# Kernel optimization log

Measured on AMD Instinct MI355X. Metric: run time of the kernel, lower is better.

## Reference

```python
import jax, jax.numpy as jnp
import numpy as np

GROUP_SIZE = 7
ROI_SCALE = 1.3
BIN_SCALE = 1.5


def setup_inputs() -> dict:
    key = jax.random.key(0)
    k1, k2, k3, k4 = jax.random.split(key, 4)
    B, C, H, W = 2, 490, 128, 128  # C = output_dim(10) * group_size(7)**2
    N = 512
    stride = 16
    features = jax.random.normal(k1, (B, C, H, W), dtype=jnp.float32)
    img_w = W * stride
    bidx = jax.random.randint(k2, (N, 1), 0, B).astype(jnp.float32)
    xy1 = jax.random.uniform(k3, (N, 2), minval=0.0, maxval=img_w - 64.0)
    wh = jax.random.uniform(k4, (N, 2), minval=32.0, maxval=512.0)
    xy2 = jnp.minimum(xy1 + wh, img_w - 1.0)
    rois = jnp.concatenate([bidx, xy1[:, 0:1], xy1[:, 1:2], xy2[:, 0:1], xy2[:, 1:2]], axis=1)
    return {"rois": rois, "features": features, "stride": stride}


def reference(rois, features, stride):
    G = GROUP_SIZE
    B, C, H, W = features.shape
    D = C // (G * G)  # output_dim, computed dynamically as in the torch module
    dt = features.dtype
    spatial_scale = 1.0 / stride

    rois = rois[:, :5].astype(dt)
    batch_idx = rois[:, 0].astype(jnp.int32)  # [N]
    # rounded roi corners in feature-map coordinates (end is inclusive +1)
    rsw = jnp.round(rois[:, 1]) * spatial_scale
    rsh = jnp.round(rois[:, 2]) * spatial_scale
    rew = (jnp.round(rois[:, 3]) + 1.0) * spatial_scale
    reh = (jnp.round(rois[:, 4]) + 1.0) * spatial_scale
    # mask (context) enlargement around roi center by ROI_SCALE
    rw, rh = rew - rsw, reh - rsh
    rwm, rhm = rw * ROI_SCALE, rh * ROI_SCALE
    swm = (rsw + rew) * 0.5 - rwm * 0.5
    shm = (rsh + reh) * 0.5 - rhm * 0.5
    rwm = jnp.maximum(rwm, 0.1)  # force tiny rois to 1x1
    rhm = jnp.maximum(rhm, 0.1)
    bin_h = rhm / G  # [N]
    bin_w = rwm / G
    dh = bin_h * (BIN_SCALE - 1.0) * 0.5  # extra bin context
    dw = bin_w * (BIN_SCALE - 1.0) * 0.5

    g = jnp.arange(G, dtype=dt)  # bin index
    hstart = jnp.clip(jnp.floor(shm[:, None] + g[None, :] * bin_h[:, None] - dh[:, None]), 0, H).astype(jnp.int32)  # [N,G]
    hend = jnp.clip(jnp.ceil(shm[:, None] + (g[None, :] + 1.0) * bin_h[:, None] + dh[:, None]), 0, H).astype(jnp.int32)
    wstart = jnp.clip(jnp.floor(swm[:, None] + g[None, :] * bin_w[:, None] - dw[:, None]), 0, W).astype(jnp.int32)
    wend = jnp.clip(jnp.ceil(swm[:, None] + (g[None, :] + 1.0) * bin_w[:, None] + dw[:, None]), 0, W).astype(jnp.int32)

    # integral image so each bin-average is 4 gathers instead of a dynamic loop
    cs = jnp.cumsum(jnp.cumsum(features, axis=2), axis=3)
    S = jnp.pad(cs, ((0, 0), (0, 0), (1, 0), (1, 0)))  # [B,C,H+1,W+1]
    # position-sensitive channel map c = (d*G + ph)*G + pw  <=>  reshape C -> [D,G,G]
    Sr = S.reshape(B, D, G, G, H + 1, W + 1)

    N = rois.shape[0]
    b_ = batch_idx[:, None, None, None]          # [N,1,1,1]
    d_ = jnp.arange(D)[None, :, None, None]      # [1,D,1,1]
    pi = jnp.arange(G)[None, None, :, None]      # [1,1,G,1] (ph)
    pj = jnp.arange(G)[None, None, None, :]      # [1,1,1,G] (pw)
    hs = hstart[:, None, :, None]
    he = hend[:, None, :, None]
    ws = wstart[:, None, None, :]
    we = wend[:, None, None, :]

    total = (Sr[b_, d_, pi, pj, he, we] - Sr[b_, d_, pi, pj, hs, we]
             - Sr[b_, d_, pi, pj, he, ws] + Sr[b_, d_, pi, pj, hs, ws])  # [N,D,G,G]

    area = ((hend - hstart)[:, None, :, None] * (wend - wstart)[:, None, None, :])  # [N,1->D,G,G] via broadcast
    area = jnp.broadcast_to(area, total.shape)
    out = jnp.where(area > 0, total / jnp.maximum(area, 1).astype(dt), jnp.zeros((), dt))
    return out
```

## Files before the change

### kernel.cpp

```cpp
#include <hip/hip_runtime.h>

#define GS   7
#define CCH  490
#define HH   128
#define WW   128
#define LDW  132
#define NB   2

__global__ __launch_bounds__(512, 4) void psroi_fused(
    const float* __restrict__ rois,
    const float* __restrict__ feat,
    const int*   __restrict__ stride_p,
    float*       __restrict__ out)
{
#pragma clang fp contract(off)
    __shared__ float S[HH * LDW];

    const int bc = blockIdx.x;
    const int b  = bc / CCH;
    const int c  = bc - b * CCH;
    const float* __restrict__ f = feat + (size_t)bc * (HH * WW);
    const int tid = threadIdx.x;

    {
        const int col = tid & 127;
        const int seg = tid >> 7;
        const int r0  = seg * 32;

        float v[32];
        const float* fp = f + r0 * WW + col;
        #pragma unroll
        for (int i = 0; i < 32; ++i)
            v[i] = fp[i * WW];
        #pragma unroll
        for (int i = 1; i < 32; ++i)
            v[i] += v[i - 1];

        S[seg * LDW + col] = v[31];
        __syncthreads();
        float off = 0.0f;
        if (seg > 0) off += S[0 * LDW + col];
        if (seg > 1) off += S[1 * LDW + col];
        if (seg > 2) off += S[2 * LDW + col];
        __syncthreads();

        float* sp = &S[r0 * LDW + col];
        #pragma unroll
        for (int i = 0; i < 32; ++i)
            sp[i * LDW] = v[i] + off;
    }
    __syncthreads();

    {
        const int row = tid >> 2;
        const int ws_ = tid & 3;
        float* rp = &S[row * LDW + ws_ * 32];

        float u[32];
        #pragma unroll
        for (int i = 0; i < 8; ++i) {
            const float4 q = *(const float4*)&rp[i * 4];
            u[4 * i + 0] = q.x; u[4 * i + 1] = q.y;
            u[4 * i + 2] = q.z; u[4 * i + 3] = q.w;
        }
        #pragma unroll
        for (int i = 1; i < 32; ++i)
            u[i] += u[i - 1];

        const float tot = u[31];
        const float t1 = __shfl_up(tot, 1, 64);
        const float t2 = __shfl_up(tot, 2, 64);
        const float t3 = __shfl_up(tot, 3, 64);
        float off = 0.0f;
        if (ws_ > 0) off += t1;
        if (ws_ > 1) off += t2;
        if (ws_ > 2) off += t3;

        #pragma unroll
        for (int i = 0; i < 8; ++i) {
            float4 q;
            q.x = u[4 * i + 0] + off; q.y = u[4 * i + 1] + off;
            q.z = u[4 * i + 2] + off; q.w = u[4 * i + 3] + off;
            *(float4*)&rp[i * 4] = q;
        }
    }
    __syncthreads();

    {
        const int n = tid;
        const float b_f = rois[n * 5 + 0];
        const int bi = (int)b_f;
        if (bi == b) {
            const float ss = 1.0f / (float)(*stride_p);
            const int d   = c / (GS * GS);
            const int rem = c - d * (GS * GS);
            const int pi  = rem / GS;
            const int pj  = rem - pi * GS;

            const float x1 = rois[n * 5 + 1];
            const float y1 = rois[n * 5 + 2];
            const float x2 = rois[n * 5 + 3];
            const float y2 = rois[n * 5 + 4];

            float rsw = rintf(x1) * ss;
            float rsh = rintf(y1) * ss;
            float rew = (rintf(x2) + 1.0f) * ss;
            float reh = (rintf(y2) + 1.0f) * ss;
            float rwv = rew - rsw;
            float rhv = reh - rsh;
            float rwm = rwv * 1.3f;
            float rhm = rhv * 1.3f;
            float swm = (rsw + rew) * 0.5f - rwm * 0.5f;
            float shm = (rsh + reh) * 0.5f - rhm * 0.5f;
            rwm = fmaxf(rwm, 0.1f);
            rhm = fmaxf(rhm, 0.1f);
            float bin_h = rhm / 7.0f;
            float bin_w = rwm / 7.0f;
            float dh = bin_h * 0.25f;
            float dw = bin_w * 0.25f;

            const float gi = (float)pi;
            const float gj = (float)pj;
            const int hs  = (int)fminf(fmaxf(floorf(shm + gi * bin_h - dh),          0.0f), 128.0f);
            const int he  = (int)fminf(fmaxf(ceilf (shm + (gi + 1.0f) * bin_h + dh), 0.0f), 128.0f);
            const int ws2 = (int)fminf(fmaxf(floorf(swm + gj * bin_w - dw),          0.0f), 128.0f);
            const int we  = (int)fminf(fmaxf(ceilf (swm + (gj + 1.0f) * bin_w + dw), 0.0f), 128.0f);

            const int area = (he - hs) * (we - ws2);
            const float A  = (he > 0 && we  > 0) ? S[(he - 1) * LDW + (we  - 1)] : 0.0f;
            const float Bv = (hs > 0 && we  > 0) ? S[(hs - 1) * LDW + (we  - 1)] : 0.0f;
            const float Cv = (he > 0 && ws2 > 0) ? S[(he - 1) * LDW + (ws2 - 1)] : 0.0f;
            const float Dv = (hs > 0 && ws2 > 0) ? S[(hs - 1) * LDW + (ws2 - 1)] : 0.0f;
            const float total = ((A - Bv) - Cv) + Dv;
            out[(size_t)n * CCH + c] = (area > 0) ? (total / (float)area) : 0.0f;
        }
    }
}

extern "C" void kernel_launch(void* const* d_in, const int* in_sizes, int n_in,
                              void* d_out, int out_size, void* d_ws, size_t ws_size,
                              hipStream_t stream)
{
    const float* rois     = (const float*)d_in[0];
    const float* feat     = (const float*)d_in[1];
    const int*   stride_p = (const int*)d_in[2];
    float*       out      = (float*)d_out;

    dim3 grid(NB * CCH);
    dim3 block(512);
    hipLaunchKernelGGL(psroi_fused, grid, block, 0, stream, rois, feat, stride_p, out);
}
```

Before: 97.78 us.

## Process both batch images per block and prefetch second image during first

Each block now handles one channel for both batch images instead of one (channel, batch) pair, halving the grid to 490 blocks. The second image's column loads are issued into registers while the first image's integral image is finished and pooled, so global loads overlap LDS work. ROI geometry is computed once and reused for both batches, and __syncthreads is replaced by an lgkmcnt wait plus a raw s_barrier. The risk is lower parallelism: 490 blocks of 512 threads may underfill the GPU, and register pressure rises because the prefetched values stay live.

```diff
diff --git a/kernel.cpp b/kernel.cpp
--- a/kernel.cpp
+++ b/kernel.cpp
@@ -5,7 +5,12 @@
 #define HH   128
 #define WW   128
 #define LDW  132
-#define NB   2
+#define HWSZ (HH * WW)
+
+__device__ __forceinline__ void bar_lds() {
+    asm volatile("s_waitcnt lgkmcnt(0)" ::: "memory");
+    __builtin_amdgcn_s_barrier();
+}
 
 __global__ __launch_bounds__(512, 4) void psroi_fused(
     const float* __restrict__ rois,
@@ -16,42 +21,65 @@
 #pragma clang fp contract(off)
     __shared__ float S[HH * LDW];
 
-    const int bc = blockIdx.x;
-    const int b  = bc / CCH;
-    const int c  = bc - b * CCH;
-    const float* __restrict__ f = feat + (size_t)bc * (HH * WW);
+    const int c   = blockIdx.x;
     const int tid = threadIdx.x;
 
+    const int col = tid & 127;
+    const int seg = tid >> 7;
+    const int r0  = seg * 32;
+
+    const float* __restrict__ f0 = feat + (size_t)c * HWSZ;
+    const float* __restrict__ f1 = feat + (size_t)(CCH + c) * HWSZ;
+
+    float v[32];
     {
-        const int col = tid & 127;
-        const int seg = tid >> 7;
-        const int r0  = seg * 32;
-
-        float v[32];
-        const float* fp = f + r0 * WW + col;
+        const float* fp = f0 + r0 * WW + col;
         #pragma unroll
         for (int i = 0; i < 32; ++i)
             v[i] = fp[i * WW];
-        #pragma unroll
-        for (int i = 1; i < 32; ++i)
-            v[i] += v[i - 1];
+    }
 
-        S[seg * LDW + col] = v[31];
-        __syncthreads();
-        float off = 0.0f;
-        if (seg > 0) off += S[0 * LDW + col];
-        if (seg > 1) off += S[1 * LDW + col];
-        if (seg > 2) off += S[2 * LDW + col];
-        __syncthreads();
+    const int n = tid;
+    const float b_f = rois[n * 5 + 0];
+    const int   bi  = (int)b_f;
+    const float ss  = 1.0f / (float)(*stride_p);
+    const int d   = c / (GS * GS);
+    const int rem = c - d * (GS * GS);
+    const int pi  = rem / GS;
+    const int pj  = rem - pi * GS;
 
-        float* sp = &S[r0 * LDW + col];
-        #pragma unroll
-        for (int i = 0; i < 32; ++i)
-            sp[i * LDW] = v[i] + off;
-    }
-    __syncthreads();
+    const float x1 = rois[n * 5 + 1];
+    const float y1 = rois[n * 5 + 2];
+    const float x2 = rois[n * 5 + 3];
+    const float y2 = rois[n * 5 + 4];
 
-    {
+    float rsw = rintf(x1) * ss;
+    float rsh = rintf(y1) * ss;
+    float rew = (rintf(x2) + 1.0f) * ss;
+    float reh = (rintf(y2) + 1.0f) * ss;
+    float rwv = rew - rsw;
+    float rhv = reh - rsh;
+    float rwm = rwv * 1.3f;
+    float rhm = rhv * 1.3f;
+    float swm = (rsw + rew) * 0.5f - rwm * 0.5f;
+    float shm = (rsh + reh) * 0.5f - rhm * 0.5f;
+    rwm = fmaxf(rwm, 0.1f);
+    rhm = fmaxf(rhm, 0.1f);
+    float bin_h = rhm / 7.0f;
+    float bin_w = rwm / 7.0f;
+    float dh = bin_h * 0.25f;
+    float dw = bin_w * 0.25f;
+
+    const float gi = (float)pi;
+    const float gj = (float)pj;
+    const int hs  = (int)fminf(fmaxf(floorf(shm + gi * bin_h - dh),          0.0f), 128.0f);
+    const int he  = (int)fminf(fmaxf(ceilf (shm + (gi + 1.0f) * bin_h + dh), 0.0f), 128.0f);
+    const int ws2 = (int)fminf(fmaxf(floorf(swm + gj * bin_w - dw),          0.0f), 128.0f);
+    const int we  = (int)fminf(fmaxf(ceilf (swm + (gj + 1.0f) * bin_w + dw), 0.0f), 128.0f);
+    const int area = (he - hs) * (we - ws2);
+
+    auto phaseB = [&]() {
+#pragma clang fp contract(off)
         const int row = tid >> 2;
         const int ws_ = tid & 3;
         float* rp = &S[row * LDW + ws_ * 32];
@@ -71,62 +99,23 @@
         const float t1 = __shfl_up(tot, 1, 64);
         const float t2 = __shfl_up(tot, 2, 64);
         const float t3 = __shfl_up(tot, 3, 64);
-        float off = 0.0f;
-        if (ws_ > 0) off += t1;
-        if (ws_ > 1) off += t2;
-        if (ws_ > 2) off += t3;
+        float off2 = 0.0f;
+        if (ws_ > 0) off2 += t1;
+        if (ws_ > 1) off2 += t2;
+        if (ws_ > 2) off2 += t3;
 
         #pragma unroll
         for (int i = 0; i < 8; ++i) {
             float4 q;
-            q.x = u[4 * i + 0] + off; q.y = u[4 * i + 1] + off;
-            q.z = u[4 * i + 2] + off; q.w = u[4 * i + 3] + off;
+            q.x = u[4 * i + 0] + off2; q.y = u[4 * i + 1] + off2;
+            q.z = u[4 * i + 2] + off2; q.w = u[4 * i + 3] + off2;
             *(float4*)&rp[i * 4] = q;
         }
-    }
-    __syncthreads();
+    };
 
-    {
-        const int n = tid;
-        const float b_f = rois[n * 5 + 0];
-        const int bi = (int)b_f;
-        if (bi == b) {
-            const float ss = 1.0f / (float)(*stride_p);
-            const int d   = c / (GS * GS);
-            const int rem = c - d * (GS * GS);
-            const int pi  = rem / GS;
-            const int pj  = rem - pi * GS;
-
-            const float x1 = rois[n * 5 + 1];
-            const float y1 = rois[n * 5 + 2];
-            const float x2 = rois[n * 5 + 3];
-            const float y2 = rois[n * 5 + 4];
-
-            float rsw = rintf(x1) * ss;
-            float rsh = rintf(y1) * ss;
-            float rew = (rintf(x2) + 1.0f) * ss;
-            float reh = (rintf(y2) + 1.0f) * ss;
-            float rwv = rew - rsw;
-            float rhv = reh - rsh;
-            float rwm = rwv * 1.3f;
-            float rhm = rhv * 1.3f;
-            float swm = (rsw + rew) * 0.5f - rwm * 0.5f;
-            float shm = (rsh + reh) * 0.5f - rhm * 0.5f;
-            rwm = fmaxf(rwm, 0.1f);
-            rhm = fmaxf(rhm, 0.1f);
-            float bin_h = rhm / 7.0f;
-            float bin_w = rwm / 7.0f;
-            float dh = bin_h * 0.25f;
-            float dw = bin_w * 0.25f;
-
-            const float gi = (float)pi;
-            const float gj = (float)pj;
-            const int hs  = (int)fminf(fmaxf(floorf(shm + gi * bin_h - dh),          0.0f), 128.0f);
-            const int he  = (int)fminf(fmaxf(ceilf (shm + (gi + 1.0f) * bin_h + dh), 0.0f), 128.0f);
-            const int ws2 = (int)fminf(fmaxf(floorf(swm + gj * bin_w - dw),          0.0f), 128.0f);
-            const int we  = (int)fminf(fmaxf(ceilf (swm + (gj + 1.0f) * bin_w + dw), 0.0f), 128.0f);
-
-            const int area = (he - hs) * (we - ws2);
+    auto pool = [&](int bsel) {
+#pragma clang fp contract(off)
+        if (bi == bsel) {
             const float A  = (he > 0 && we  > 0) ? S[(he - 1) * LDW + (we  - 1)] : 0.0f;
             const float Bv = (hs > 0 && we  > 0) ? S[(hs - 1) * LDW + (we  - 1)] : 0.0f;
             const float Cv = (he > 0 && ws2 > 0) ? S[(he - 1) * LDW + (ws2 - 1)] : 0.0f;
@@ -134,7 +123,54 @@
             const float total = ((A - Bv) - Cv) + Dv;
             out[(size_t)n * CCH + c] = (area > 0) ? (total / (float)area) : 0.0f;
         }
+    };
+
+    #pragma unroll
+    for (int i = 1; i < 32; ++i) v[i] += v[i - 1];
+    S[seg * LDW + col] = v[31];
+    bar_lds();
+    {
+        float off = 0.0f;
+        if (seg > 0) off += S[0 * LDW + col];
+        if (seg > 1) off += S[1 * LDW + col];
+        if (seg > 2) off += S[2 * LDW + col];
+        bar_lds();
+        float* sp = &S[r0 * LDW + col];
+        #pragma unroll
+        for (int i = 0; i < 32; ++i)
+            sp[i * LDW] = v[i] + off;
     }
+    {
+        const float* fp = f1 + r0 * WW + col;
+        #pragma unroll
+        for (int i = 0; i < 32; ++i)
+            v[i] = fp[i * WW];
+    }
+    bar_lds();
+    phaseB();
+    bar_lds();
+    pool(0);
+    bar_lds();
+
+    #pragma unroll
+    for (int i = 1; i < 32; ++i) v[i] += v[i - 1];
+    S[seg * LDW + col] = v[31];
+    bar_lds();
+    {
+        float off = 0.0f;
+        if (seg > 0) off += S[0 * LDW + col];
+        if (seg > 1) off += S[1 * LDW + col];
+        if (seg > 2) off += S[2 * LDW + col];
+        bar_lds();
+        float* sp = &S[r0 * LDW + col];
+        #pragma unroll
+        for (int i = 0; i < 32; ++i)
+            sp[i * LDW] = v[i] + off;
+    }
+    bar_lds();
+    phaseB();
+    bar_lds();
+    pool(1);
 }
 
 extern "C" void kernel_launch(void* const* d_in, const int* in_sizes, int n_in,
@@ -146,7 +182,7 @@
     const int*   stride_p = (const int*)d_in[2];
     float*       out      = (float*)d_out;
 
-    dim3 grid(NB * CCH);
+    dim3 grid(CCH);
     dim3 block(512);
     hipLaunchKernelGGL(psroi_fused, grid, block, 0, stream, rois, feat, stride_p, out);
 }
```

Result: slower. 99.82 us (+2.1%).
